# Optimization experiments

Hardware: AMD Instinct MI355X
Metric: run time of the kernel (lower is better)

The kernel has to match this reference:

```python
import jax, jax.numpy as jnp
import numpy as np

EPS = 1e-10
NCLASSES, NENT, NREL, D, ANON = 8192, 4096, 256, 128, 4
B = 8


def setup_inputs() -> dict:
    key = jax.random.key(0)
    ks = jax.random.split(key, 7)
    # xavier-ish init scales for the tables / linear
    s_emb = float(np.sqrt(2.0 / (NENT + D)))
    return {
        "x": jax.random.randint(ks[0], (B, 2), 0, NREL),  # col0: relation id, col1: class id
        "anon_e_emb": jax.random.normal(ks[1], (ANON, D), dtype=jnp.float32) * 0.05,
        "c_table": jax.random.normal(ks[2], (NCLASSES, D), dtype=jnp.float32) * s_emb,
        "r_table": jax.random.normal(ks[3], (NREL, D), dtype=jnp.float32) * s_emb,
        "e_table": jax.random.normal(ks[4], (NENT, D), dtype=jnp.float32) * s_emb,
        "fc_w": jax.random.normal(ks[5], (1, 2 * D), dtype=jnp.float32) * float(np.sqrt(2.0 / (2 * D + 1))),
        "fc_b": jnp.zeros((1,), dtype=jnp.float32),
    }


def reference(x, anon_e_emb, c_table, r_table, e_table, fc_w, fc_b):
    # FALCON exists-restriction path with product t-norm and max measure.
    # fc_0(cat(l, r)) is decomposed exactly: W @ cat(l,r) = w1.l + w2.r (+ b),
    # avoiding the O(B*N^2*2d) concat tensor of the original.
    d = e_table.shape[-1]
    w1 = fc_w[0, :d]   # weights on the first (class / left-entity) half
    w2 = fc_w[0, d:]   # weights on the second (entity) half
    b = fc_b[0]

    e_all = jnp.concatenate([e_table, anon_e_emb], axis=0)  # [N, d], N = nentities + anon_e
    r_emb = r_table[x[:, 0]]                                # [B, d]
    c_emb = c_table[x[:, 1]]                                # [B, d]

    # _get_c_fs_batch: c_fs[b, j] = sigmoid(w1.c[b] + w2.e[j] + b)
    c_fs = jax.nn.sigmoid((c_emb @ w1)[:, None] + (e_all @ w2)[None, :] + b)  # [B, N]

    # _get_r_fs_batch: r_fs[b, i, j] = sigmoid(w1.(e[j] + r[b]) + w2.e[i] + b)
    aj = (e_all @ w1)[None, :] + (r_emb @ w1)[:, None] + b  # [B, N] (varies over j)
    ci = e_all @ w2                                         # [N]    (varies over i)
    r_fs = jax.nn.sigmoid(aj[:, None, :] + ci[None, :, None])  # [B, N, N]

    # _logical_exist with product t-norm: max_j (r_fs * c_fs)
    fs = jnp.max(r_fs * c_fs[:, None, :], axis=-1)  # [B, N]

    # get_cc_loss (max_measure='max'), mean over batch
    loss = jnp.mean(-jnp.log(1.0 - jnp.max(fs, axis=-1) + EPS))
    return loss
```

## Files before the change

kernel.cpp:

```cpp
#include <hip/hip_runtime.h>
#include <math.h>

#define E_ALL  4100
#define NENT_C 4096
#define DIM    128
#define NBLK_UV 129

__global__ __launch_bounds__(256)
void k_uv(const float* __restrict__ e_table,
          const float* __restrict__ anon,
          const float* __restrict__ fc_w,
          float* __restrict__ u, float* __restrict__ v,
          float* __restrict__ pbv)
{
    const int lane = threadIdx.x & 63;
    const int wave = threadIdx.x >> 6;
    __shared__ float s_wv[4];

    const float w1a = fc_w[2*lane];
    const float w1b = fc_w[2*lane + 1];
    const float w2a = fc_w[DIM + 2*lane];
    const float w2b = fc_w[DIM + 2*lane + 1];

    const int jbase = blockIdx.x * 32 + wave * 8;
    float wvmax = -INFINITY;
#pragma unroll
    for (int r = 0; r < 8; ++r) {
        const int j = jbase + r;
        if (j >= E_ALL) break;
        const float* row = (j < NENT_C) ? (e_table + (size_t)j * DIM)
                                        : (anon + (size_t)(j - NENT_C) * DIM);
        const float2 e = *reinterpret_cast<const float2*>(row + 2*lane);
        float pu = fmaf(e.x, w1a, e.y * w1b);
        float pv = fmaf(e.x, w2a, e.y * w2b);
#pragma unroll
        for (int o = 32; o; o >>= 1) {
            pu += __shfl_xor(pu, o);
            pv += __shfl_xor(pv, o);
        }
        if (lane == 0) {
            u[j] = pu;
            v[j] = pv;
            wvmax = fmaxf(wvmax, pv);
        }
    }
    if (lane == 0) s_wv[wave] = wvmax;
    __syncthreads();
    if (threadIdx.x == 0)
        pbv[blockIdx.x] = fmaxf(fmaxf(s_wv[0], s_wv[1]), fmaxf(s_wv[2], s_wv[3]));
}

__global__ __launch_bounds__(1024)
void k_final(const float* __restrict__ u, const float* __restrict__ v,
             const float* __restrict__ pbv,
             const int* __restrict__ x,
             const float* __restrict__ c_table,
             const float* __restrict__ r_table,
             const float* __restrict__ fc_w,
             const float* __restrict__ fc_b,
             float* __restrict__ out)
{
    __shared__ float s_vmax, s_sr[8], s_sc[8];
    __shared__ float s_q[8][16];
    const int tid  = threadIdx.x;
    const int lane = tid & 63;
    const int wave = tid >> 6;

    {
        const float w1a = fc_w[2*lane];
        const float w1b = fc_w[2*lane + 1];
        const float* src;
        if (wave < 8) src = r_table + (size_t)x[2*wave] * DIM;
        else          src = c_table + (size_t)x[2*(wave - 8) + 1] * DIM;
        const float2 t = *reinterpret_cast<const float2*>(src + 2*lane);
        float p = fmaf(t.x, w1a, t.y * w1b);
#pragma unroll
        for (int o = 32; o; o >>= 1) p += __shfl_xor(p, o);
        if (lane == 0) {
            if (wave < 8) s_sr[wave] = p;
            else          s_sc[wave - 8] = p;
        }
    }
    if (wave == 0) {
        float vm = -INFINITY;
        for (int i = lane; i < NBLK_UV; i += 64) vm = fmaxf(vm, pbv[i]);
#pragma unroll
        for (int o = 32; o; o >>= 1) vm = fmaxf(vm, __shfl_xor(vm, o));
        if (lane == 0) s_vmax = vm;
    }
    __syncthreads();

    const float b0   = fc_b[0];
    const float vmax = s_vmax;
    float A[8], C[8], q[8];
#pragma unroll
    for (int b = 0; b < 8; ++b) {
        A[b] = s_sr[b] + b0 + vmax;
        C[b] = s_sc[b] + b0;
        q[b] = INFINITY;
    }

    for (int j = tid; j < E_ALL; j += 1024) {
        const float uj = u[j];
        const float vj = v[j];
#pragma unroll
        for (int b = 0; b < 8; ++b) {
            const float e1 = __expf(-(uj + A[b]));
            const float e2 = __expf(-(vj + C[b]));
            q[b] = fminf(q[b], (1.0f + e1) * (1.0f + e2));
        }
    }

#pragma unroll
    for (int b = 0; b < 8; ++b) {
        float t = q[b];
#pragma unroll
        for (int o = 32; o; o >>= 1) t = fminf(t, __shfl_xor(t, o));
        if (lane == 0) s_q[b][wave] = t;
    }
    __syncthreads();
    if (tid < 8) {
        float qm = INFINITY;
#pragma unroll
        for (int w = 0; w < 16; ++w) qm = fminf(qm, s_q[tid][w]);
        const float fs = 1.0f / qm;
        float t = -logf(1.0f - fs + 1e-10f);
#pragma unroll
        for (int o = 4; o; o >>= 1) t += __shfl_xor(t, o);
        if (tid == 0) out[0] = t * 0.125f;
    }
}

extern "C" void kernel_launch(void* const* d_in, const int* in_sizes, int n_in,
                              void* d_out, int out_size, void* d_ws, size_t ws_size,
                              hipStream_t stream) {
    const int*   x        = (const int*)d_in[0];
    const float* anon     = (const float*)d_in[1];
    const float* c_table  = (const float*)d_in[2];
    const float* r_table  = (const float*)d_in[3];
    const float* e_table  = (const float*)d_in[4];
    const float* fc_w     = (const float*)d_in[5];
    const float* fc_b     = (const float*)d_in[6];
    float* out = (float*)d_out;

    float* u   = (float*)d_ws;
    float* v   = u + 4224;
    float* pbv = v + 4224;

    k_uv<<<NBLK_UV, 256, 0, stream>>>(e_table, anon, fc_w, u, v, pbv);
    k_final<<<1, 1024, 0, stream>>>(u, v, pbv, x, c_table, r_table, fc_w, fc_b, out);
}
```

Baseline: 17.25 us.

## Hoist exponentials out of batch loop, pack u/v, widen row loads

The first kernel now uses half-waves with float4 loads to process two rows at once, issuing all row loads before reducing. It writes u and v interleaved as float2. The final kernel prefetches all u/v pairs up front and factors exp(-(u+A)) into exp(-u)*exp(-A), so only two exponentials per entity are computed instead of sixteen. This cuts transcendental work and load latency, at the cost of small rounding differences and hard-coded trip counts.

```diff
diff --git a/kernel.cpp b/kernel.cpp
--- a/kernel.cpp
+++ b/kernel.cpp
@@ -1,58 +1,68 @@
 #include <hip/hip_runtime.h>
 #include <math.h>
 
-#define E_ALL  4100
-#define NENT_C 4096
-#define DIM    128
+#define E_ALL   4100
+#define NENT_C  4096
+#define DIM     128
 #define NBLK_UV 129
 
 __global__ __launch_bounds__(256)
 void k_uv(const float* __restrict__ e_table,
           const float* __restrict__ anon,
           const float* __restrict__ fc_w,
-          float* __restrict__ u, float* __restrict__ v,
+          float2* __restrict__ uv,
           float* __restrict__ pbv)
 {
-    const int lane = threadIdx.x & 63;
-    const int wave = threadIdx.x >> 6;
-    __shared__ float s_wv[4];
+    const int tid  = threadIdx.x;
+    const int lane = tid & 63;
+    const int half = lane >> 5;
+    const int l32  = lane & 31;
+    const int wave = tid >> 6;
+    __shared__ float s_wv[8];
 
-    const float w1a = fc_w[2*lane];
-    const float w1b = fc_w[2*lane + 1];
-    const float w2a = fc_w[DIM + 2*lane];
-    const float w2b = fc_w[DIM + 2*lane + 1];
+    const float4 w1q = *reinterpret_cast<const float4*>(fc_w + 4*l32);
+    const float4 w2q = *reinterpret_cast<const float4*>(fc_w + DIM + 4*l32);
 
     const int jbase = blockIdx.x * 32 + wave * 8;
+
+    float4 e[4];
+#pragma unroll
+    for (int i = 0; i < 4; ++i) {
+        int j  = jbase + 2*i + half;
+        int jc = (j < E_ALL) ? j : (E_ALL - 1);
+        const float* row = (jc < NENT_C) ? (e_table + (size_t)jc * DIM)
+                                         : (anon + (size_t)(jc - NENT_C) * DIM);
+        e[i] = *reinterpret_cast<const float4*>(row + 4*l32);
+    }
+
     float wvmax = -INFINITY;
 #pragma unroll
-    for (int r = 0; r < 8; ++r) {
-        const int j = jbase + r;
-        if (j >= E_ALL) break;
-        const float* row = (j < NENT_C) ? (e_table + (size_t)j * DIM)
-                                        : (anon + (size_t)(j - NENT_C) * DIM);
-        const float2 e = *reinterpret_cast<const float2*>(row + 2*lane);
-        float pu = fmaf(e.x, w1a, e.y * w1b);
-        float pv = fmaf(e.x, w2a, e.y * w2b);
+    for (int i = 0; i < 4; ++i) {
+        const int j = jbase + 2*i + half;
+        float pu = fmaf(e[i].x, w1q.x, fmaf(e[i].y, w1q.y, fmaf(e[i].z, w1q.z, e[i].w * w1q.w)));
+        float pv = fmaf(e[i].x, w2q.x, fmaf(e[i].y, w2q.y, fmaf(e[i].z, w2q.z, e[i].w * w2q.w)));
 #pragma unroll
-        for (int o = 32; o; o >>= 1) {
+        for (int o = 16; o; o >>= 1) {
             pu += __shfl_xor(pu, o);
             pv += __shfl_xor(pv, o);
         }
-        if (lane == 0) {
-            u[j] = pu;
-            v[j] = pv;
+        if (l32 == 0 && j < E_ALL) {
+            uv[j] = make_float2(pu, pv);
             wvmax = fmaxf(wvmax, pv);
         }
     }
-    if (lane == 0) s_wv[wave] = wvmax;
+    if (l32 == 0) s_wv[wave * 2 + half] = wvmax;
     __syncthreads();
-    if (threadIdx.x == 0)
-        pbv[blockIdx.x] = fmaxf(fmaxf(s_wv[0], s_wv[1]), fmaxf(s_wv[2], s_wv[3]));
+    if (tid == 0) {
+        float bm = s_wv[0];
+#pragma unroll
+        for (int k = 1; k < 8; ++k) bm = fmaxf(bm, s_wv[k]);
+        pbv[blockIdx.x] = bm;
+    }
 }
 
 __global__ __launch_bounds__(1024)
-void k_final(const float* __restrict__ u, const float* __restrict__ v,
-             const float* __restrict__ pbv,
+void k_final(const float2* __restrict__ uv, const float* __restrict__ pbv,
              const int* __restrict__ x,
              const float* __restrict__ c_table,
              const float* __restrict__ r_table,
@@ -66,12 +76,17 @@
     const int lane = tid & 63;
     const int wave = tid >> 6;
 
+    const float2 p0 = uv[tid];
+    const float2 p1 = uv[tid + 1024];
+    const float2 p2 = uv[tid + 2048];
+    const float2 p3 = uv[tid + 3072];
+    const float2 p4 = uv[(tid < 4) ? tid + 4096 : tid];
+
     {
         const float w1a = fc_w[2*lane];
         const float w1b = fc_w[2*lane + 1];
-        const float* src;
-        if (wave < 8) src = r_table + (size_t)x[2*wave] * DIM;
-        else          src = c_table + (size_t)x[2*(wave - 8) + 1] * DIM;
+        const float* src = (wave < 8) ? (r_table + (size_t)x[2*wave] * DIM)
+                                      : (c_table + (size_t)x[2*(wave - 8) + 1] * DIM);
         const float2 t = *reinterpret_cast<const float2*>(src + 2*lane);
         float p = fmaf(t.x, w1a, t.y * w1b);
 #pragma unroll
@@ -82,8 +97,10 @@
         }
     }
     if (wave == 0) {
-        float vm = -INFINITY;
-        for (int i = lane; i < NBLK_UV; i += 64) vm = fmaxf(vm, pbv[i]);
+        const float a = pbv[lane];
+        const float b = pbv[lane + 64];
+        const float c = pbv[128];
+        float vm = fmaxf(fmaxf(a, b), c);
 #pragma unroll
         for (int o = 32; o; o >>= 1) vm = fmaxf(vm, __shfl_xor(vm, o));
         if (lane == 0) s_vmax = vm;
@@ -92,24 +109,27 @@
 
     const float b0   = fc_b[0];
     const float vmax = s_vmax;
-    float A[8], C[8], q[8];
+    float kb[8], mb[8], q[8];
 #pragma unroll
     for (int b = 0; b < 8; ++b) {
-        A[b] = s_sr[b] + b0 + vmax;
-        C[b] = s_sc[b] + b0;
-        q[b] = INFINITY;
+        kb[b] = __expf(-(s_sr[b] + b0 + vmax));
+        mb[b] = __expf(-(s_sc[b] + b0));
+        q[b]  = INFINITY;
     }
 
-    for (int j = tid; j < E_ALL; j += 1024) {
-        const float uj = u[j];
-        const float vj = v[j];
-#pragma unroll
-        for (int b = 0; b < 8; ++b) {
-            const float e1 = __expf(-(uj + A[b]));
-            const float e2 = __expf(-(vj + C[b]));
-            q[b] = fminf(q[b], (1.0f + e1) * (1.0f + e2));
-        }
+#define PROC(P)                                                   \
+    {                                                             \
+        const float eu = __expf(-(P).x);                          \
+        const float ev = __expf(-(P).y);                          \
+        _Pragma("unroll")                                         \
+        for (int b = 0; b < 8; ++b) {                             \
+            const float t1 = fmaf(eu, kb[b], 1.0f);               \
+            const float t2 = fmaf(ev, mb[b], 1.0f);               \
+            q[b] = fminf(q[b], t1 * t2);                          \
+        }                                                         \
     }
+    PROC(p0); PROC(p1); PROC(p2); PROC(p3); PROC(p4);
+#undef PROC
 
 #pragma unroll
     for (int b = 0; b < 8; ++b) {
@@ -143,10 +163,9 @@
     const float* fc_b     = (const float*)d_in[6];
     float* out = (float*)d_out;
 
-    float* u   = (float*)d_ws;
-    float* v   = u + 4224;
-    float* pbv = v + 4224;
+    float2* uv  = (float2*)d_ws;
+    float*  pbv = (float*)d_ws + 8320;
 
-    k_uv<<<NBLK_UV, 256, 0, stream>>>(e_table, anon, fc_w, u, v, pbv);
-    k_final<<<1, 1024, 0, stream>>>(u, v, pbv, x, c_table, r_table, fc_w, fc_b, out);
+    k_uv<<<NBLK_UV, 256, 0, stream>>>(e_table, anon, fc_w, uv, pbv);
+    k_final<<<1, 1024, 0, stream>>>(uv, pbv, x, c_table, r_table, fc_w, fc_b, out);
 }
```

Result: faster. 14.82 us (-14.1%).
